# Optimization experiments

Hardware: AMD Instinct MI355X
Metric: run time of the kernel (lower is better)

## Reference

```python
import jax, jax.numpy as jnp
import numpy as np

BN_EPS = 1e-5

def setup_inputs() -> dict:
    key = jax.random.key(0)
    ks = jax.random.split(key, 8)
    B, N, d_in, d_out, M, K = 16, 16384, 64, 128, 4096, 16
    pos = jax.random.normal(ks[0], (B, N, 3), dtype=jnp.float32)
    feat = jax.random.normal(ks[1], (B, N, d_in), dtype=jnp.float32)
    fps_preprocess = jax.random.randint(ks[2], (B, M), 0, N, dtype=jnp.int64)
    k_idx = jax.random.randint(ks[3], (B, M, K), 0, N, dtype=jnp.int64)
    W = jax.random.normal(ks[4], (d_out, d_in), dtype=jnp.float32) / np.sqrt(d_in)
    b = jax.random.normal(ks[5], (d_out,), dtype=jnp.float32) * 0.01
    gamma = jnp.ones((d_out,), dtype=jnp.float32)
    beta = jnp.zeros((d_out,), dtype=jnp.float32)
    return {"pos": pos, "feat": feat, "fps_preprocess": fps_preprocess,
            "k_idx": k_idx, "W": W, "b": b, "gamma": gamma, "beta": beta}

def reference(pos, feat, fps_preprocess, k_idx, W, b, gamma, beta):
    B = pos.shape[0]
    # Linear: [B,N,d_in] @ [d_in,d_out] -> [B,N,d_out]
    h = jnp.einsum('bnd,od->bno', feat, W) + b
    # BatchNorm1d over channels (batch stats, biased variance) + ReLU
    mu = jnp.mean(h, axis=(0, 1))
    var = jnp.mean(jnp.square(h - mu), axis=(0, 1))
    h = jax.nn.relu(gamma * (h - mu) * jax.lax.rsqrt(var + BN_EPS) + beta)
    # Downsample positions via FPS indices: [B,M,3]
    pos_ds = jnp.take_along_axis(pos, fps_preprocess[:, :, None], axis=1)
    # Batched kNN gather [B,M,K,d_out] then max over neighbors
    bidx = jnp.arange(B)[:, None, None]
    feat_knn = h[bidx, k_idx]            # [B,M,K,d_out]
    feat_ds = jnp.max(feat_knn, axis=2)  # [B,M,d_out]
    return (pos_ds, feat_ds)
```

## Files before the change

### kernel.cpp

```cpp
#include <hip/hip_runtime.h>
#include <hip/hip_bf16.h>
#include <stdint.h>

typedef float f4 __attribute__((ext_vector_type(4)));
typedef float f32x4v __attribute__((ext_vector_type(4)));
typedef float f32x16 __attribute__((ext_vector_type(16)));
typedef short bf16x8 __attribute__((ext_vector_type(8)));
typedef unsigned int u32x2 __attribute__((ext_vector_type(2)));

static constexpr int Bc = 16, Nc = 16384, DIN = 64, DOUT = 128, Mc = 4096, KNN = 16;
static constexpr long Rr = (long)Bc * Nc;
static constexpr float EPS = 1e-5f;
static constexpr int POS_OUT = Bc * Mc * 3;
static constexpr int GBLK = 512;
static constexpr int PSTRIDE = 4160;
static constexpr int RGRP = 32;
static constexpr int CG_STRIDE = 8224;

__device__ __forceinline__ uint32_t cvt2(float a, float b) {
    union { __hip_bfloat162 h; uint32_t u; } c;
    c.h = __float22bfloat162_rn(make_float2(a, b));
    return c.u;
}
__device__ __forceinline__ bf16x8 mkfrag(f4 x0, f4 x1) {
    union { uint32_t u[4]; bf16x8 v; } r;
    r.u[0] = cvt2(x0[0], x0[1]);
    r.u[1] = cvt2(x0[2], x0[3]);
    r.u[2] = cvt2(x1[0], x1[1]);
    r.u[3] = cvt2(x1[2], x1[3]);
    return r.v;
}

__global__ __launch_bounds__(256) void k_gram(const float* __restrict__ feat,
                                              unsigned short* __restrict__ feat16,
                                              float* __restrict__ part)
{
    __shared__ alignas(16) char lds[4 * CG_STRIDE];
    const int t = threadIdx.x;
    const int lane = t & 63;
    const int w = t >> 6;
    const long R0 = (long)blockIdx.x * 512;
    const f4* feat4 = (const f4*)feat;
    const unsigned lds_base = (unsigned)(size_t)&lds[0];

    f32x4v acc[4][4];
#pragma unroll
    for (int mi = 0; mi < 4; ++mi)
#pragma unroll
        for (int mj = 0; mj < 4; ++mj) acc[mi][mj] = (f32x4v){0.f, 0.f, 0.f, 0.f};
    f4 csum = (f4){0.f, 0.f, 0.f, 0.f};

    f4 v[16];
#pragma unroll
    for (int i = 0; i < 16; ++i)
        v[i] = feat4[R0 * 16 + t + i * 256];

    const int c4 = t & 15;
    const int cg = c4 >> 2;

    for (int ch = 0; ch < 2; ++ch) {
#pragma unroll
        for (int i = 0; i < 16; ++i) {
            int row = (t + i * 256) >> 4;
            uint2 pk = {cvt2(v[i][0], v[i][1]), cvt2(v[i][2], v[i][3])};
            csum += v[i];
            *(uint2*)(feat16 + (size_t)(R0 + ch * 256 + row) * 64 + c4 * 4) = pk;
            *(uint2*)(lds + cg * CG_STRIDE + row * 32 + (c4 & 3) * 8) = pk;
        }
        __syncthreads();
        if (ch == 0) {
#pragma unroll
            for (int i = 0; i < 16; ++i)
                v[i] = feat4[(R0 + 256) * 16 + t + i * 256];
        }
#pragma unroll
        for (int s = 0; s < 2; ++s) {
            const unsigned base = lds_base + (unsigned)((w * 2 + s) * 32 * 32 + lane * 8);
            u32x2 r0[4], r1[4];
#pragma unroll
            for (int g = 0; g < 4; ++g) {
                unsigned a = base + g * CG_STRIDE;
                asm volatile("ds_read_b64_tr_b16 %0, %2 offset:0\n\t"
                             "ds_read_b64_tr_b16 %1, %2 offset:512"
                             : "=v"(r0[g]), "=v"(r1[g]) : "v"(a));
            }
            asm volatile("s_waitcnt lgkmcnt(0)" ::: "memory");
            __builtin_amdgcn_sched_barrier(0);
            bf16x8 f[4];
#pragma unroll
            for (int g = 0; g < 4; ++g) {
                union { u32x2 p[2]; bf16x8 v8; } u;
                u.p[0] = r0[g]; u.p[1] = r1[g];
                f[g] = u.v8;
            }
#pragma unroll
            for (int mi = 0; mi < 4; ++mi)
#pragma unroll
                for (int mj = 0; mj < 4; ++mj)
                    acc[mi][mj] = __builtin_amdgcn_mfma_f32_16x16x32_bf16(
                        f[mi], f[mj], acc[mi][mj], 0, 0, 0);
        }
        __syncthreads();
    }

    float* fbuf = (float*)lds;
    ((f4*)fbuf)[t] = csum;
    __syncthreads();
    float* pb = part + (size_t)blockIdx.x * PSTRIDE;
    if (t < 16) {
        f4 s = (f4){0.f, 0.f, 0.f, 0.f};
#pragma unroll
        for (int q = 0; q < 16; ++q) s += ((f4*)fbuf)[q * 16 + t];
        ((f4*)pb)[t] = s;
    }
    __syncthreads();
    float* buf = fbuf + (w & 1) * 4096;
    const int lcol = lane & 15, lrow4 = (lane >> 4) * 4;
    if (w < 2) {
#pragma unroll
        for (int mi = 0; mi < 4; ++mi)
#pragma unroll
            for (int mj = 0; mj < 4; ++mj)
#pragma unroll
                for (int rg = 0; rg < 4; ++rg)
                    buf[(mi * 16 + lrow4 + rg) * 64 + mj * 16 + lcol] = acc[mi][mj][rg];
    }
    __syncthreads();
    if (w >= 2) {
#pragma unroll
        for (int mi = 0; mi < 4; ++mi)
#pragma unroll
            for (int mj = 0; mj < 4; ++mj)
#pragma unroll
                for (int rg = 0; rg < 4; ++rg)
                    buf[(mi * 16 + lrow4 + rg) * 64 + mj * 16 + lcol] += acc[mi][mj][rg];
    }
    __syncthreads();
#pragma unroll
    for (int q = 0; q < 16; ++q) {
        int e = t + q * 256;
        pb[64 + e] = fbuf[e] + fbuf[4096 + e];
    }
}

__global__ __launch_bounds__(256) void k_reduce1(const float* __restrict__ part,
                                                 float* __restrict__ part2)
{
    const int gid = blockIdx.x * 256 + threadIdx.x;
    const int grp = blockIdx.y;
    if (gid >= PSTRIDE) return;
    const float* pp = part + (size_t)grp * (GBLK / RGRP) * PSTRIDE + gid;
    float s[8];
#pragma unroll
    for (int j = 0; j < 8; ++j) s[j] = 0.f;
#pragma unroll
    for (int i = 0; i < GBLK / RGRP; i += 8)
#pragma unroll
        for (int j = 0; j < 8; ++j)
            s[j] += pp[(size_t)(i + j) * PSTRIDE];
    part2[(size_t)grp * PSTRIDE + gid] =
        ((s[0] + s[1]) + (s[2] + s[3])) + ((s[4] + s[5]) + (s[6] + s[7]));
}

__global__ __launch_bounds__(256) void k_reduce2(const float* __restrict__ part2,
                                                 float* __restrict__ stats)
{
    const int gid = blockIdx.x * 256 + threadIdx.x;
    if (gid >= PSTRIDE) return;
    float s[8];
#pragma unroll
    for (int j = 0; j < 8; ++j) s[j] = 0.f;
#pragma unroll
    for (int i = 0; i < RGRP; i += 8)
#pragma unroll
        for (int j = 0; j < 8; ++j)
            s[j] += part2[(size_t)(i + j) * PSTRIDE + gid];
    stats[gid] = ((s[0] + s[1]) + (s[2] + s[3])) + ((s[4] + s[5]) + (s[6] + s[7]));
}

__global__ __launch_bounds__(256) void k_gram_at(const float* __restrict__ feat,
                                                 float* __restrict__ stats)
{
    __shared__ float tile[64 * 64];
    f4* tile4 = (f4*)tile;
    const f4* feat4 = (const f4*)feat;
    const int t = threadIdx.x;
    const int i0 = (t >> 4) << 2;
    const int j0 = (t & 15) << 2;
    float acc[16];
#pragma unroll
    for (int k = 0; k < 16; ++k) acc[k] = 0.f;
    float csum = 0.f;
    for (int c = 0; c < 8; ++c) {
        const int base4 = (blockIdx.x * 512 + c * 64) * 16;
        __syncthreads();
#pragma unroll
        for (int k = 0; k < 4; ++k) tile4[t + k * 256] = feat4[base4 + t + k * 256];
        __syncthreads();
        for (int r = 0; r < 64; ++r) {
            f4 fi = tile4[r * 16 + (i0 >> 2)];
            f4 fj = tile4[r * 16 + (j0 >> 2)];
#pragma unroll
            for (int ii = 0; ii < 4; ++ii)
#pragma unroll
                for (int jj = 0; jj < 4; ++jj)
                    acc[ii * 4 + jj] = fmaf(fi[ii], fj[jj], acc[ii * 4 + jj]);
        }
        if (t < 64) {
            for (int r = 0; r < 64; ++r) csum += tile[r * 64 + t];
        }
    }
#pragma unroll
    for (int ii = 0; ii < 4; ++ii)
#pragma unroll
        for (int jj = 0; jj < 4; ++jj)
            atomicAdd(&stats[64 + (i0 + ii) * 64 + (j0 + jj)], acc[ii * 4 + jj]);
    if (t < 64) atomicAdd(&stats[t], csum);
}

__global__ __launch_bounds__(64) void k_stats(const float* __restrict__ stats,
                                              const float* __restrict__ W,
                                              const float* __restrict__ gamma,
                                              const float* __restrict__ beta,
                                              float* __restrict__ ST)
{
    const int o = blockIdx.x;
    const int i = threadIdx.x;
    __shared__ float wrow[64];
    wrow[i] = W[o * 64 + i];
    __syncthreads();
    const float* G = stats + 64;
    float inner = 0.f;
    for (int j = 0; j < 64; ++j) inner = fmaf(G[i * 64 + j], wrow[j], inner);
    float qi = inner * wrow[i];
    float cwi = stats[i] * wrow[i];
#pragma unroll
    for (int off = 32; off > 0; off >>= 1) {
        qi += __shfl_down(qi, off);
        cwi += __shfl_down(cwi, off);
    }
    if (i == 0) {
        const double invR = 1.0 / (double)Rr;
        double meanr = (double)cwi * invR;
        double var = (double)qi * invR - meanr * meanr;
        float s = gamma[o] / sqrtf((float)var + EPS);
        ST[o] = s;
        ST[DOUT + o] = beta[o] - (float)meanr * s;
    }
}

__global__ __launch_bounds__(512) void k_gmax(const unsigned short* __restrict__ feat16,
                                              const float* __restrict__ W,
                                              const float* __restrict__ ST,
                                              const int* __restrict__ kidx,
                                              const int* __restrict__ fps,
                                              const float* __restrict__ pos,
                                              float* __restrict__ out)
{
    __shared__ char lW[16 * 1024];
    const int t = threadIdx.x;
    const f4* W4 = (const f4*)W;
#pragma unroll
    for (int i = 0; i < 4; ++i) {
        int idx = t + i * 512;
        int row = idx >> 4, c4 = idx & 15;
        f4 v = W4[idx];
        uint2 pk = {cvt2(v[0], v[1]), cvt2(v[2], v[3])};
        *(uint2*)(lW + row * 128 + ((c4 * 8) ^ ((row & 7) << 4))) = pk;
    }

    const int lane = t & 63;
    const int w = t >> 6;
    const int l31 = lane & 31;
    const int hi = lane >> 5;

    const int bl = blockIdx.x;
    const int j = bl >> 3;
    const int batch = (bl & 7) + 8 * (j >> 7);
    const int p0 = batch * Mc + (j & 127) * 32 + w * 4;

    int ids[2];
#pragma unroll
    for (int it = 0; it < 2; ++it)
        ids[it] = __builtin_nontemporal_load(&kidx[(p0 + 2 * it) * KNN + l31]);

    __syncthreads();

    const unsigned short* fb = feat16 + (size_t)batch * Nc * 64 + hi * 8;
    bf16x8 A[2][4];
#pragma unroll
    for (int it = 0; it < 2; ++it) {
        const unsigned short* rp = fb + (size_t)ids[it] * 64;
        A[it][0] = *(const bf16x8*)(rp);
        A[it][1] = *(const bf16x8*)(rp + 16);
        A[it][2] = *(const bf16x8*)(rp + 32);
        A[it][3] = *(const bf16x8*)(rp + 48);
    }

    if (l31 < 3) {
#pragma unroll
        for (int it = 0; it < 2; ++it) {
            int p = p0 + 2 * it + hi;
            int id2 = fps[p];
            __builtin_nontemporal_store(pos[((size_t)batch * Nc + id2) * 3 + l31],
                                        &out[p * 3 + l31]);
        }
    }

#pragma unroll
    for (int cgh = 0; cgh < 2; ++cgh) {
        bf16x8 wf[2][4];
#pragma unroll
        for (int cc = 0; cc < 2; ++cc) {
            int row = cgh * 64 + cc * 32 + l31;
#pragma unroll
            for (int ks = 0; ks < 4; ++ks)
                wf[cc][ks] = *(const bf16x8*)(lW + row * 128 +
                                              ((ks * 32 + hi * 16) ^ ((row & 7) << 4)));
        }
#pragma unroll
        for (int it = 0; it < 2; ++it) {
#pragma unroll
            for (int cc = 0; cc < 2; ++cc) {
                const int cg = cgh * 2 + cc;
                f32x16 acc = {};
                __builtin_amdgcn_s_setprio(1);
#pragma unroll
                for (int ks = 0; ks < 4; ++ks)
                    acc = __builtin_amdgcn_mfma_f32_32x32x16_bf16(A[it][ks], wf[cc][ks], acc, 0, 0, 0);
                __builtin_amdgcn_s_setprio(0);
                float vmA = fmaxf(fmaxf(fmaxf(acc[0], acc[1]), fmaxf(acc[2], acc[3])),
                                  fmaxf(fmaxf(acc[4], acc[5]), fmaxf(acc[6], acc[7])));
                float vmB = fmaxf(fmaxf(fmaxf(acc[8], acc[9]), fmaxf(acc[10], acc[11])),
                                  fmaxf(fmaxf(acc[12], acc[13]), fmaxf(acc[14], acc[15])));
                vmA = fmaxf(vmA, __shfl_xor(vmA, 32));
                vmB = fmaxf(vmB, __shfl_xor(vmB, 32));
                float vsel = hi ? vmB : vmA;
                float sc = ST[cg * 32 + l31];
                float tc = ST[DOUT + cg * 32 + l31];
                __builtin_nontemporal_store(
                    fmaxf(fmaf(vsel, sc, tc), 0.f),
                    &out[POS_OUT + (size_t)(p0 + 2 * it + hi) * DOUT + cg * 32 + l31]);
            }
        }
    }
}

__global__ __launch_bounds__(128) void k_gather_rc(const float* __restrict__ feat,
                                                   const float* __restrict__ W,
                                                   const float* __restrict__ ST,
                                                   const int* __restrict__ kidx,
                                                   const int* __restrict__ fps,
                                                   const float* __restrict__ pos,
                                                   float* __restrict__ out)
{
    __shared__ float frow[KNN][DIN];
    const int p = blockIdx.x;
    const int o = threadIdx.x;
    const int b = p >> 12;
    const f4* featf = (const f4*)feat;
    f4* frow4 = (f4*)frow;
#pragma unroll
    for (int q = 0; q < 2; ++q) {
        int jj = o + q * 128;
        int row = jj >> 4, i4 = jj & 15;
        int id = kidx[p * KNN + row];
        frow4[jj] = featf[((size_t)b * Nc + id) * 16 + i4];
    }
    __syncthreads();
    float wreg[64];
#pragma unroll
    for (int i4 = 0; i4 < 16; ++i4) {
        f4 wv = ((const f4*)W)[o * 16 + i4];
        wreg[i4 * 4 + 0] = wv[0];
        wreg[i4 * 4 + 1] = wv[1];
        wreg[i4 * 4 + 2] = wv[2];
        wreg[i4 * 4 + 3] = wv[3];
    }
    const float s = ST[o], tt = ST[DOUT + o];
    float vm = 0.f;
    for (int k = 0; k < KNN; ++k) {
        float acc = 0.f;
#pragma unroll
        for (int i = 0; i < 64; ++i) acc = fmaf(frow[k][i], wreg[i], acc);
        vm = fmaxf(vm, fmaf(acc, s, tt));
    }
    out[POS_OUT + (size_t)p * DOUT + o] = vm;
    if (o < 3) {
        int id = fps[p];
        out[p * 3 + o] = pos[((size_t)b * Nc + id) * 3 + o];
    }
}

extern "C" void kernel_launch(void* const* d_in, const int* in_sizes, int n_in,
                              void* d_out, int out_size, void* d_ws, size_t ws_size,
                              hipStream_t stream)
{
    const float* pos   = (const float*)d_in[0];
    const float* feat  = (const float*)d_in[1];
    const int*   fps   = (const int*)d_in[2];
    const int*   kidx  = (const int*)d_in[3];
    const float* W     = (const float*)d_in[4];
    const float* gamma = (const float*)d_in[6];
    const float* beta  = (const float*)d_in[7];
    float* out = (float*)d_out;

    float* stats = (float*)d_ws;
    float* ST = stats + PSTRIDE;
    const size_t F16_OFF = 32768;
    const size_t F16_BYTES = (size_t)Rr * DIN * 2;
    unsigned short* feat16 = (unsigned short*)((char*)d_ws + F16_OFF);
    float* part  = (float*)((char*)d_ws + F16_OFF + F16_BYTES);
    float* part2 = part + (size_t)GBLK * PSTRIDE;
    const size_t need = F16_OFF + F16_BYTES +
                        (size_t)(GBLK + RGRP) * PSTRIDE * 4;

    if (ws_size >= need) {
        k_gram<<<GBLK, 256, 0, stream>>>(feat, feat16, part);
        k_reduce1<<<dim3((PSTRIDE + 255) / 256, RGRP), 256, 0, stream>>>(part, part2);
        k_reduce2<<<(PSTRIDE + 255) / 256, 256, 0, stream>>>(part2, stats);
        k_stats<<<DOUT, 64, 0, stream>>>(stats, W, gamma, beta, ST);
        k_gmax<<<2048, 512, 0, stream>>>(feat16, W, ST, kidx, fps, pos, out);
    } else {
        hipMemsetAsync(d_ws, 0, PSTRIDE * 4, stream);
        k_gram_at<<<512, 256, 0, stream>>>(feat, stats);
        k_stats<<<DOUT, 64, 0, stream>>>(stats, W, gamma, beta, ST);
        k_gather_rc<<<Bc * Mc, 128, 0, stream>>>(feat, W, ST, kidx, fps, pos, out);
    }
}
```

Measured before the change: 68.00 us.

## Restructure gather-max kernel with register-resident bf16 W and prefetched neighbor rows

W is now converted to bf16 once in k_stats and held in registers by k_gmax, instead of every block staging it through LDS with a barrier. The MFMA row mapping is rearranged so that each half-wave holds all 16 neighbors of one point. That lets the max over neighbors finish within a lane without cross-lane shuffles. Each wave now loops over four point-pairs and prefetches the next kidx and feature rows while the current MFMAs run, at the cost of more VGPRs and a smaller 256-thread block.

Result: slower. 81.51 us (+19.9%).

```diff
diff --git a/kernel.cpp b/kernel.cpp
--- a/kernel.cpp
+++ b/kernel.cpp
@@ -21,14 +21,6 @@
     union { __hip_bfloat162 h; uint32_t u; } c;
     c.h = __float22bfloat162_rn(make_float2(a, b));
     return c.u;
-}
-__device__ __forceinline__ bf16x8 mkfrag(f4 x0, f4 x1) {
-    union { uint32_t u[4]; bf16x8 v; } r;
-    r.u[0] = cvt2(x0[0], x0[1]);
-    r.u[1] = cvt2(x0[2], x0[3]);
-    r.u[2] = cvt2(x1[0], x1[1]);
-    r.u[3] = cvt2(x1[2], x1[3]);
-    return r.v;
 }
 
 __global__ __launch_bounds__(256) void k_gram(const float* __restrict__ feat,
@@ -222,12 +214,14 @@
                                               const float* __restrict__ W,
                                               const float* __restrict__ gamma,
                                               const float* __restrict__ beta,
-                                              float* __restrict__ ST)
+                                              float* __restrict__ ST,
+                                              unsigned short* __restrict__ W16)
 {
     const int o = blockIdx.x;
     const int i = threadIdx.x;
     __shared__ float wrow[64];
     wrow[i] = W[o * 64 + i];
+    W16[o * 64 + i] = (unsigned short)(cvt2(wrow[i], wrow[i]) & 0xffffu);
     __syncthreads();
     const float* G = stats + 64;
     float inner = 0.f;
@@ -249,100 +243,93 @@
     }
 }
 
-__global__ __launch_bounds__(512) void k_gmax(const unsigned short* __restrict__ feat16,
-                                              const float* __restrict__ W,
+__global__ __launch_bounds__(256) void k_gmax(const unsigned short* __restrict__ feat16,
+                                              const unsigned short* __restrict__ W16,
                                               const float* __restrict__ ST,
                                               const int* __restrict__ kidx,
                                               const int* __restrict__ fps,
                                               const float* __restrict__ pos,
                                               float* __restrict__ out)
 {
-    __shared__ char lW[16 * 1024];
     const int t = threadIdx.x;
-    const f4* W4 = (const f4*)W;
-#pragma unroll
-    for (int i = 0; i < 4; ++i) {
-        int idx = t + i * 512;
-        int row = idx >> 4, c4 = idx & 15;
-        f4 v = W4[idx];
-        uint2 pk = {cvt2(v[0], v[1]), cvt2(v[2], v[3])};
-        *(uint2*)(lW + row * 128 + ((c4 * 8) ^ ((row & 7) << 4))) = pk;
-    }
-
     const int lane = t & 63;
     const int w = t >> 6;
     const int l31 = lane & 31;
     const int hi = lane >> 5;
 
+    bf16x8 wf[4][4];
+#pragma unroll
+    for (int cg = 0; cg < 4; ++cg)
+#pragma unroll
+        for (int ks = 0; ks < 4; ++ks)
+            wf[cg][ks] = *(const bf16x8*)(W16 + (size_t)(cg * 32 + l31) * 64 +
+                                          ks * 16 + hi * 8);
+    float sc[4], tc[4];
+#pragma unroll
+    for (int cg = 0; cg < 4; ++cg) {
+        sc[cg] = ST[cg * 32 + l31];
+        tc[cg] = ST[DOUT + cg * 32 + l31];
+    }
+
     const int bl = blockIdx.x;
     const int j = bl >> 3;
     const int batch = (bl & 7) + 8 * (j >> 7);
-    const int p0 = batch * Mc + (j & 127) * 32 + w * 4;
-
-    int ids[2];
-#pragma unroll
-    for (int it = 0; it < 2; ++it)
-        ids[it] = __builtin_nontemporal_load(&kidx[(p0 + 2 * it) * KNN + l31]);
-
-    __syncthreads();
+    const int g0 = (j & 127) * 16 + w * 4;
+
+    const int prsel = (l31 >> 2) & 1;
+    const int ksel = (l31 & 3) + ((l31 >> 3) << 2);
 
     const unsigned short* fb = feat16 + (size_t)batch * Nc * 64 + hi * 8;
-    bf16x8 A[2][4];
-#pragma unroll
-    for (int it = 0; it < 2; ++it) {
-        const unsigned short* rp = fb + (size_t)ids[it] * 64;
-        A[it][0] = *(const bf16x8*)(rp);
-        A[it][1] = *(const bf16x8*)(rp + 16);
-        A[it][2] = *(const bf16x8*)(rp + 32);
-        A[it][3] = *(const bf16x8*)(rp + 48);
-    }
-
-    if (l31 < 3) {
-#pragma unroll
-        for (int it = 0; it < 2; ++it) {
-            int p = p0 + 2 * it + hi;
+
+    int p0 = batch * Mc + g0 * 2;
+    int id = __builtin_nontemporal_load(&kidx[(p0 + prsel) * KNN + ksel]);
+
+    bf16x8 A[4];
+    {
+        const unsigned short* rp = fb + (size_t)id * 64;
+#pragma unroll
+        for (int ks = 0; ks < 4; ++ks) A[ks] = *(const bf16x8*)(rp + ks * 16);
+    }
+
+#pragma unroll
+    for (int i = 0; i < 4; ++i) {
+        const int pcur = p0;
+        int idn = 0;
+        if (i < 3) {
+            p0 += 2;
+            idn = __builtin_nontemporal_load(&kidx[(p0 + prsel) * KNN + ksel]);
+        }
+        float vm[4];
+#pragma unroll
+        for (int cg = 0; cg < 4; ++cg) {
+            f32x16 acc = {};
+            __builtin_amdgcn_s_setprio(1);
+#pragma unroll
+            for (int ks = 0; ks < 4; ++ks)
+                acc = __builtin_amdgcn_mfma_f32_32x32x16_bf16(A[ks], wf[cg][ks], acc, 0, 0, 0);
+            __builtin_amdgcn_s_setprio(0);
+            float a = fmaxf(fmaxf(acc[0], acc[1]), fmaxf(acc[2], acc[3]));
+            float b = fmaxf(fmaxf(acc[4], acc[5]), fmaxf(acc[6], acc[7]));
+            float c = fmaxf(fmaxf(acc[8], acc[9]), fmaxf(acc[10], acc[11]));
+            float d = fmaxf(fmaxf(acc[12], acc[13]), fmaxf(acc[14], acc[15]));
+            vm[cg] = fmaxf(fmaxf(a, b), fmaxf(c, d));
+        }
+        if (i < 3) {
+            const unsigned short* rp = fb + (size_t)idn * 64;
+#pragma unroll
+            for (int ks = 0; ks < 4; ++ks) A[ks] = *(const bf16x8*)(rp + ks * 16);
+        }
+        if (l31 < 3) {
+            int p = pcur + hi;
             int id2 = fps[p];
             __builtin_nontemporal_store(pos[((size_t)batch * Nc + id2) * 3 + l31],
                                         &out[p * 3 + l31]);
         }
-    }
-
-#pragma unroll
-    for (int cgh = 0; cgh < 2; ++cgh) {
-        bf16x8 wf[2][4];
-#pragma unroll
-        for (int cc = 0; cc < 2; ++cc) {
-            int row = cgh * 64 + cc * 32 + l31;
-#pragma unroll
-            for (int ks = 0; ks < 4; ++ks)
-                wf[cc][ks] = *(const bf16x8*)(lW + row * 128 +
-                                              ((ks * 32 + hi * 16) ^ ((row & 7) << 4)));
-        }
-#pragma unroll
-        for (int it = 0; it < 2; ++it) {
-#pragma unroll
-            for (int cc = 0; cc < 2; ++cc) {
-                const int cg = cgh * 2 + cc;
-                f32x16 acc = {};
-                __builtin_amdgcn_s_setprio(1);
-#pragma unroll
-                for (int ks = 0; ks < 4; ++ks)
-                    acc = __builtin_amdgcn_mfma_f32_32x32x16_bf16(A[it][ks], wf[cc][ks], acc, 0, 0, 0);
-                __builtin_amdgcn_s_setprio(0);
-                float vmA = fmaxf(fmaxf(fmaxf(acc[0], acc[1]), fmaxf(acc[2], acc[3])),
-                                  fmaxf(fmaxf(acc[4], acc[5]), fmaxf(acc[6], acc[7])));
-                float vmB = fmaxf(fmaxf(fmaxf(acc[8], acc[9]), fmaxf(acc[10], acc[11])),
-                                  fmaxf(fmaxf(acc[12], acc[13]), fmaxf(acc[14], acc[15])));
-                vmA = fmaxf(vmA, __shfl_xor(vmA, 32));
-                vmB = fmaxf(vmB, __shfl_xor(vmB, 32));
-                float vsel = hi ? vmB : vmA;
-                float sc = ST[cg * 32 + l31];
-                float tc = ST[DOUT + cg * 32 + l31];
-                __builtin_nontemporal_store(
-                    fmaxf(fmaf(vsel, sc, tc), 0.f),
-                    &out[POS_OUT + (size_t)(p0 + 2 * it + hi) * DOUT + cg * 32 + l31]);
-            }
-        }
+#pragma unroll
+        for (int cg = 0; cg < 4; ++cg)
+            __builtin_nontemporal_store(
+                fmaxf(fmaf(vm[cg], sc[cg], tc[cg]), 0.f),
+                &out[POS_OUT + (size_t)(pcur + hi) * DOUT + cg * 32 + l31]);
     }
 }
 
@@ -407,7 +394,8 @@
 
     float* stats = (float*)d_ws;
     float* ST = stats + PSTRIDE;
-    const size_t F16_OFF = 32768;
+    unsigned short* W16 = (unsigned short*)((char*)d_ws + 20480);
+    const size_t F16_OFF = 49152;
     const size_t F16_BYTES = (size_t)Rr * DIN * 2;
     unsigned short* feat16 = (unsigned short*)((char*)d_ws + F16_OFF);
     float* part  = (float*)((char*)d_ws + F16_OFF + F16_BYTES);
@@ -419,12 +407,12 @@
         k_gram<<<GBLK, 256, 0, stream>>>(feat, feat16, part);
         k_reduce1<<<dim3((PSTRIDE + 255) / 256, RGRP), 256, 0, stream>>>(part, part2);
         k_reduce2<<<(PSTRIDE + 255) / 256, 256, 0, stream>>>(part2, stats);
-        k_stats<<<DOUT, 64, 0, stream>>>(stats, W, gamma, beta, ST);
-        k_gmax<<<2048, 512, 0, stream>>>(feat16, W, ST, kidx, fps, pos, out);
+        k_stats<<<DOUT, 64, 0, stream>>>(stats, W, gamma, beta, ST, W16);
+        k_gmax<<<2048, 256, 0, stream>>>(feat16, W16, ST, kidx, fps, pos, out);
     } else {
         hipMemsetAsync(d_ws, 0, PSTRIDE * 4, stream);
         k_gram_at<<<512, 256, 0, stream>>>(feat, stats);
-        k_stats<<<DOUT, 64, 0, stream>>>(stats, W, gamma, beta, ST);
+        k_stats<<<DOUT, 64, 0, stream>>>(stats, W, gamma, beta, ST, W16);
         k_gather_rc<<<Bc * Mc, 128, 0, stream>>>(feat, W, ST, kidx, fps, pos, out);
     }
 }
```
